# Kernel tuning notes

Hardware: AMD Instinct MI355X
Metric: run time of the kernel (lower is better)

## Reference

```python
import jax, jax.numpy as jnp
import numpy as np

N_NODES = 100000
DIM = 128
N_REL = 3
N_EDGES = 500000


def setup_inputs() -> dict:
    key = jax.random.key(0)
    k1, k2, k3, k4 = jax.random.split(key, 4)
    node_embeds = jax.random.normal(k1, (N_NODES, DIM), dtype=jnp.float32)
    rel_emb = jax.random.normal(k2, (N_REL, DIM), dtype=jnp.float32)
    src_idx = jax.random.randint(k3, (N_REL, N_EDGES), 0, N_NODES, dtype=jnp.int64)
    dst_idx = jax.random.randint(k4, (N_REL, N_EDGES), 0, N_NODES, dtype=jnp.int64)
    return {"node_embeds": node_embeds, "rel_emb": rel_emb,
            "src_idx": src_idx, "dst_idx": dst_idx}


def reference(node_embeds, rel_emb, src_idx, dst_idx):
    # DistMult per-edge score, per edge type r:
    #   score[r, e] = sum_d x[src[r,e], d] * x[dst[r,e], d] * rel[r, d]
    # Faithful to: u_mul_v gather+mul, then mv with relation embedding,
    # vectorized over the etype loop.
    xs = node_embeds[src_idx]  # [R, E, d]
    xd = node_embeds[dst_idx]  # [R, E, d]
    scores = jnp.einsum('red,red,rd->re', xs, xd, rel_emb)  # [R, E]
    return scores
```

## Files before the change

kernel.cpp:

```cpp
#include <hip/hip_runtime.h>

#define DIM 128

__global__ __launch_bounds__(256) void quant_kernel(
    const float* __restrict__ x,
    unsigned* __restrict__ qt,
    float* __restrict__ scales,
    int rows)
{
    const int lane = threadIdx.x & 31;
    const int rpb  = blockDim.x >> 5;
    int row        = blockIdx.x * rpb + (threadIdx.x >> 5);
    const int strd = gridDim.x * rpb;

    for (; row < rows; row += strd) {
        float4 v = ((const float4*)(x + (size_t)row * DIM))[lane];
        float m = fmaxf(fmaxf(fabsf(v.x), fabsf(v.y)),
                        fmaxf(fabsf(v.z), fabsf(v.w)));
        m = fmaxf(m, __shfl_xor(m, 16));
        m = fmaxf(m, __shfl_xor(m, 8));
        m = fmaxf(m, __shfl_xor(m, 4));
        m = fmaxf(m, __shfl_xor(m, 2));
        m = fmaxf(m, __shfl_xor(m, 1));
        const float inv = (m > 0.f) ? 127.f / m : 0.f;
        const float sc  = (m > 0.f) ? m / 127.f : 0.f;
        int q0 = (int)rintf(v.x * inv);
        int q1 = (int)rintf(v.y * inv);
        int q2 = (int)rintf(v.z * inv);
        int q3 = (int)rintf(v.w * inv);
        unsigned pk = ((unsigned)q0 & 0xffu)
                    | (((unsigned)q1 & 0xffu) << 8)
                    | (((unsigned)q2 & 0xffu) << 16)
                    | (((unsigned)q3 & 0xffu) << 24);
        qt[(size_t)row * 32 + lane] = pk;
        if (lane == 0) scales[row] = sc;
    }
}

__device__ __forceinline__ float dot4_i8(unsigned a, unsigned b, float4 c) {
    int a0 = (int)(a << 24) >> 24, b0 = (int)(b << 24) >> 24;
    int a1 = (int)(a << 16) >> 24, b1 = (int)(b << 16) >> 24;
    int a2 = (int)(a <<  8) >> 24, b2 = (int)(b <<  8) >> 24;
    int a3 = (int)a         >> 24, b3 = (int)b         >> 24;
    return (float)(a0 * b0) * c.x + (float)(a1 * b1) * c.y
         + (float)(a2 * b2) * c.z + (float)(a3 * b3) * c.w;
}

__global__ __launch_bounds__(256) void distmult_i8_kernel(
    const unsigned* __restrict__ qt,
    const float* __restrict__ scales,
    const float* __restrict__ rel,
    const int* __restrict__ src,
    const int* __restrict__ dst,
    float* __restrict__ out,
    int n_edges)
{
    const int r    = blockIdx.y;
    const int lane = threadIdx.x & 7;
    const int gpb  = blockDim.x >> 3;

    const float* cR = rel + (size_t)r * DIM + lane * 16;
    const float4 c0 = ((const float4*)cR)[0];
    const float4 c1 = ((const float4*)cR)[1];
    const float4 c2 = ((const float4*)cR)[2];
    const float4 c3 = ((const float4*)cR)[3];

    const int* srcR = src + (size_t)r * n_edges;
    const int* dstR = dst + (size_t)r * n_edges;
    float*     outR = out + (size_t)r * n_edges;

    int e      = blockIdx.x * gpb + (threadIdx.x >> 3);
    int stride = gridDim.x * gpb;

    for (; e < n_edges; e += stride) {
        int s = __builtin_nontemporal_load(srcR + e);
        int d = __builtin_nontemporal_load(dstR + e);
        uint4 a = *(const uint4*)(qt + (size_t)s * 32 + lane * 4);
        uint4 b = *(const uint4*)(qt + (size_t)d * 32 + lane * 4);
        float p = dot4_i8(a.x, b.x, c0) + dot4_i8(a.y, b.y, c1)
                + dot4_i8(a.z, b.z, c2) + dot4_i8(a.w, b.w, c3);
        p += __shfl_xor(p, 4);
        p += __shfl_xor(p, 2);
        p += __shfl_xor(p, 1);
        if (lane == 0) {
            float v = p * scales[s] * scales[d];
            __builtin_nontemporal_store(v, outR + e);
        }
    }
}

__global__ __launch_bounds__(256) void distmult_f32_kernel(
    const float* __restrict__ x,
    const float* __restrict__ rel,
    const int* __restrict__ src,
    const int* __restrict__ dst,
    float* __restrict__ out,
    int n_edges)
{
    const int r    = blockIdx.y;
    const int lane = threadIdx.x & 31;
    const int gpb  = blockDim.x >> 5;

    const float4 c = ((const float4*)(rel + (size_t)r * DIM))[lane];
    const int*  srcR = src + (size_t)r * n_edges;
    const int*  dstR = dst + (size_t)r * n_edges;
    float*      outR = out + (size_t)r * n_edges;

    int e      = blockIdx.x * gpb + (threadIdx.x >> 5);
    int stride = gridDim.x * gpb;

    for (; e < n_edges; e += stride) {
        int s = srcR[e];
        int d = dstR[e];
        float4 a = ((const float4*)(x + (size_t)s * DIM))[lane];
        float4 b = ((const float4*)(x + (size_t)d * DIM))[lane];
        float p = a.x * b.x * c.x + a.y * b.y * c.y
                + a.z * b.z * c.z + a.w * b.w * c.w;
        p += __shfl_xor(p, 16);
        p += __shfl_xor(p, 8);
        p += __shfl_xor(p, 4);
        p += __shfl_xor(p, 2);
        p += __shfl_xor(p, 1);
        if (lane == 0) outR[e] = p;
    }
}

extern "C" void kernel_launch(void* const* d_in, const int* in_sizes, int n_in,
                              void* d_out, int out_size, void* d_ws, size_t ws_size,
                              hipStream_t stream) {
    const float* x   = (const float*)d_in[0];
    const float* rel = (const float*)d_in[1];
    const int*   src = (const int*)d_in[2];
    const int*   dst = (const int*)d_in[3];
    float*       out = (float*)d_out;

    const int n_rel   = in_sizes[1] / DIM;
    const int n_edges = in_sizes[2] / n_rel;
    const int rows    = in_sizes[0] / DIM;

    const size_t qt_bytes = (size_t)rows * DIM;
    const size_t sc_bytes = (size_t)rows * sizeof(float);
    dim3 grid(2048, n_rel);

    if (ws_size >= qt_bytes + sc_bytes) {
        unsigned* qt     = (unsigned*)d_ws;
        float*    scales = (float*)((char*)d_ws + qt_bytes);
        quant_kernel<<<2048, 256, 0, stream>>>(x, qt, scales, rows);
        distmult_i8_kernel<<<grid, 256, 0, stream>>>(
            qt, scales, rel, src, dst, out, n_edges);
    } else {
        distmult_f32_kernel<<<grid, 256, 0, stream>>>(x, rel, src, dst, out, n_edges);
    }
}
```

Baseline: 67.19 us.

## Bucket edges by source range before int8 gather for cache locality

Adds count, scan and scatter passes that partition each relation's edges into 8 buckets by source node range, packing src, dst and edge id into 64-bit records. The gather kernel then processes one bucket per block group, so source-row reads hit a smaller working set in cache. The cost is four extra kernel launches, a pass over the indices with shared and global atomics, and a scattered output write pattern.

```diff
diff --git a/kernel.cpp b/kernel.cpp
--- a/kernel.cpp
+++ b/kernel.cpp
@@ -1,6 +1,8 @@
 #include <hip/hip_runtime.h>
 
 #define DIM 128
+#define SRC_BITS 17
+#define EID_SHIFT 34
 
 __global__ __launch_bounds__(256) void quant_kernel(
     const float* __restrict__ x,
@@ -37,6 +39,110 @@
     }
 }
 
+__device__ __forceinline__ int bucket_of(int s, float inv8) {
+    return min(7, (int)((float)s * inv8));
+}
+
+__global__ void zero_kernel(unsigned* __restrict__ counts, int n) {
+    int i = threadIdx.x;
+    if (i < n) counts[i] = 0u;
+}
+
+__global__ __launch_bounds__(256) void count_kernel(
+    const int* __restrict__ src, int n_edges, float inv8,
+    unsigned* __restrict__ counts)
+{
+    const int r = blockIdx.y;
+    __shared__ unsigned h[8];
+    if (threadIdx.x < 8) h[threadIdx.x] = 0u;
+    __syncthreads();
+
+    const int* srcR = src + (size_t)r * n_edges;
+    int e = blockIdx.x * blockDim.x + threadIdx.x;
+    const int stride = gridDim.x * blockDim.x;
+    for (; e < n_edges; e += stride) {
+        int s = __builtin_nontemporal_load(srcR + e);
+        atomicAdd(&h[bucket_of(s, inv8)], 1u);
+    }
+    __syncthreads();
+    if (threadIdx.x < 8 && h[threadIdx.x])
+        atomicAdd(&counts[r * 8 + threadIdx.x], h[threadIdx.x]);
+}
+
+__global__ void scan_kernel(const unsigned* __restrict__ counts,
+                            unsigned* __restrict__ offsets,
+                            unsigned* __restrict__ cursors, int nbins) {
+    if (threadIdx.x == 0 && blockIdx.x == 0) {
+        unsigned acc = 0;
+        for (int i = 0; i < nbins; ++i) {
+            offsets[i] = acc;
+            cursors[i] = acc;
+            acc += counts[i];
+        }
+        offsets[nbins] = acc;
+    }
+}
+
+__global__ __launch_bounds__(256) void scatter_kernel(
+    const int* __restrict__ src, const int* __restrict__ dst,
+    int n_edges, float inv8,
+    unsigned long long* __restrict__ rec,
+    unsigned* __restrict__ cursors)
+{
+    const int r   = blockIdx.y;
+    const int tid = threadIdx.x;
+    __shared__ unsigned lcnt[8];
+    __shared__ unsigned lbase[8];
+
+    const int* srcR = src + (size_t)r * n_edges;
+    const int* dstR = dst + (size_t)r * n_edges;
+    unsigned*  curR = cursors + r * 8;
+
+    const int step = gridDim.x * blockDim.x * 2;
+    for (int base = blockIdx.x * blockDim.x * 2; base < n_edges; base += step) {
+        if (tid < 8) lcnt[tid] = 0u;
+        __syncthreads();
+
+        const int e0 = base + tid * 2;
+        const int e1 = e0 + 1;
+        const bool v0 = e0 < n_edges;
+        const bool v1 = e1 < n_edges;
+        int s0 = 0, d0 = 0, b0 = 0, s1 = 0, d1 = 0, b1 = 0;
+        unsigned r0 = 0, r1 = 0;
+        if (v0) {
+            s0 = __builtin_nontemporal_load(srcR + e0);
+            d0 = __builtin_nontemporal_load(dstR + e0);
+            b0 = bucket_of(s0, inv8);
+            r0 = atomicAdd(&lcnt[b0], 1u);
+        }
+        if (v1) {
+            s1 = __builtin_nontemporal_load(srcR + e1);
+            d1 = __builtin_nontemporal_load(dstR + e1);
+            b1 = bucket_of(s1, inv8);
+            r1 = atomicAdd(&lcnt[b1], 1u);
+        }
+        __syncthreads();
+        if (tid < 8) {
+            unsigned c = lcnt[tid];
+            lbase[tid] = c ? atomicAdd(&curR[tid], c) : 0u;
+        }
+        __syncthreads();
+        if (v0) {
+            unsigned long long pk = (unsigned long long)(unsigned)s0
+                                  | ((unsigned long long)(unsigned)d0 << SRC_BITS)
+                                  | ((unsigned long long)(unsigned)e0 << EID_SHIFT);
+            __builtin_nontemporal_store(pk, &rec[lbase[b0] + r0]);
+        }
+        if (v1) {
+            unsigned long long pk = (unsigned long long)(unsigned)s1
+                                  | ((unsigned long long)(unsigned)d1 << SRC_BITS)
+                                  | ((unsigned long long)(unsigned)e1 << EID_SHIFT);
+            __builtin_nontemporal_store(pk, &rec[lbase[b1] + r1]);
+        }
+        __syncthreads();
+    }
+}
+
 __device__ __forceinline__ float dot4_i8(unsigned a, unsigned b, float4 c) {
     int a0 = (int)(a << 24) >> 24, b0 = (int)(b << 24) >> 24;
     int a1 = (int)(a << 16) >> 24, b1 = (int)(b << 16) >> 24;
@@ -44,6 +150,53 @@
     int a3 = (int)a         >> 24, b3 = (int)b         >> 24;
     return (float)(a0 * b0) * c.x + (float)(a1 * b1) * c.y
          + (float)(a2 * b2) * c.z + (float)(a3 * b3) * c.w;
+}
+
+__global__ __launch_bounds__(256) void distmult_i8_bucketed_kernel(
+    const unsigned* __restrict__ qt,
+    const float* __restrict__ scales,
+    const float* __restrict__ rel,
+    const unsigned long long* __restrict__ rec,
+    const unsigned* __restrict__ offsets,
+    float* __restrict__ out,
+    int n_edges)
+{
+    const int r    = blockIdx.y;
+    const int lane = threadIdx.x & 7;
+    const int gpb  = blockDim.x >> 3;
+    const int b    = r * 8 + (blockIdx.x & 7);
+
+    const float* cR = rel + (size_t)r * DIM + lane * 16;
+    const float4 c0 = ((const float4*)cR)[0];
+    const float4 c1 = ((const float4*)cR)[1];
+    const float4 c2 = ((const float4*)cR)[2];
+    const float4 c3 = ((const float4*)cR)[3];
+
+    float* outR = out + (size_t)r * n_edges;
+
+    const int lo = (int)offsets[b];
+    const int hi = (int)offsets[b + 1];
+    int i = lo + (int)(blockIdx.x >> 3) * gpb + (threadIdx.x >> 3);
+    const int stride = (int)(gridDim.x >> 3) * gpb;
+
+    for (; i < hi; i += stride) {
+        unsigned long long rc = __builtin_nontemporal_load(rec + i);
+        int s = (int)(rc & ((1u << SRC_BITS) - 1));
+        int d = (int)((rc >> SRC_BITS) & ((1u << SRC_BITS) - 1));
+        int e = (int)(rc >> EID_SHIFT);
+
+        uint4 a  = *(const uint4*)(qt + (size_t)s * 32 + lane * 4);
+        uint4 bb = *(const uint4*)(qt + (size_t)d * 32 + lane * 4);
+        float p = dot4_i8(a.x, bb.x, c0) + dot4_i8(a.y, bb.y, c1)
+                + dot4_i8(a.z, bb.z, c2) + dot4_i8(a.w, bb.w, c3);
+        p += __shfl_xor(p, 4);
+        p += __shfl_xor(p, 2);
+        p += __shfl_xor(p, 1);
+        if (lane == 0) {
+            float v = p * scales[s] * scales[d];
+            __builtin_nontemporal_store(v, outR + e);
+        }
+    }
 }
 
 __global__ __launch_bounds__(256) void distmult_i8_kernel(
@@ -138,11 +291,43 @@
     const int n_edges = in_sizes[2] / n_rel;
     const int rows    = in_sizes[0] / DIM;
 
-    const size_t qt_bytes = (size_t)rows * DIM;
-    const size_t sc_bytes = (size_t)rows * sizeof(float);
+    const size_t qt_bytes  = (size_t)rows * DIM;
+    const size_t sc_bytes  = (size_t)rows * sizeof(float);
+    size_t rec_off = qt_bytes + sc_bytes;
+    rec_off = (rec_off + 7) & ~(size_t)7;
+    const size_t rec_bytes  = (size_t)n_rel * n_edges * sizeof(unsigned long long);
+    const size_t meta_off   = rec_off + rec_bytes;
+    const size_t meta_bytes = 256 * sizeof(unsigned);
+
     dim3 grid(2048, n_rel);
 
-    if (ws_size >= qt_bytes + sc_bytes) {
+    const bool can_i8 = ws_size >= qt_bytes + sc_bytes;
+    const bool can_bucket = can_i8
+        && ws_size >= meta_off + meta_bytes
+        && rows    <= (1 << SRC_BITS)
+        && n_edges <= (1 << (64 - EID_SHIFT - 45 >= 0 ? 19 : 19))
+        && n_edges <= 524288
+        && n_rel   <= 8;
+
+    if (can_bucket) {
+        unsigned*           qt      = (unsigned*)d_ws;
+        float*              scales  = (float*)((char*)d_ws + qt_bytes);
+        unsigned long long* rec     = (unsigned long long*)((char*)d_ws + rec_off);
+        unsigned*           counts  = (unsigned*)((char*)d_ws + meta_off);
+        unsigned*           offsets = counts + 64;
+        unsigned*           cursors = counts + 160;
+        const int   nbins = n_rel * 8;
+        const float inv8  = 8.0f / (float)rows;
+
+        quant_kernel<<<2048, 256, 0, stream>>>(x, qt, scales, rows);
+        zero_kernel<<<1, 64, 0, stream>>>(counts, nbins);
+        count_kernel<<<dim3(256, n_rel), 256, 0, stream>>>(src, n_edges, inv8, counts);
+        scan_kernel<<<1, 1, 0, stream>>>(counts, offsets, cursors, nbins);
+        scatter_kernel<<<dim3(512, n_rel), 256, 0, stream>>>(src, dst, n_edges, inv8,
+                                                             rec, cursors);
+        distmult_i8_bucketed_kernel<<<grid, 256, 0, stream>>>(
+            qt, scales, rel, rec, offsets, out, n_edges);
+    } else if (can_i8) {
         unsigned* qt     = (unsigned*)d_ws;
         float*    scales = (float*)((char*)d_ws + qt_bytes);
         quant_kernel<<<2048, 256, 0, stream>>>(x, qt, scales, rows);
```

Result: slower. 121.8 us (+81.2%).
